# Kernel tuning notes

Hardware: AMD Instinct MI355X
Metric: run time of the kernel (lower is better)

The kernel has to match this reference:

```python
import jax, jax.numpy as jnp
import numpy as np

DIM = 1024

def setup_inputs() -> dict:
    key = jax.random.key(0)
    k1, k2, k3, k4, k5 = jax.random.split(key, 5)
    B, Sq, Skv = 8, 2048, 2048
    x = jax.random.normal(k1, (B, Sq, DIM), dtype=jnp.float32)
    context = jax.random.normal(k2, (B, Skv, DIM), dtype=jnp.float32)
    # nn.Linear default init scale ~ uniform; use scaled normal for stability
    s = DIM ** -0.5
    Wq = jax.random.normal(k3, (DIM, DIM), dtype=jnp.float32) * s
    Wk = jax.random.normal(k4, (DIM, DIM), dtype=jnp.float32) * s
    Wv = jax.random.normal(k5, (DIM, DIM), dtype=jnp.float32) * s
    return {"x": x, "context": context, "Wq": Wq, "Wk": Wk, "Wv": Wv}

def reference(x, context, Wq, Wk, Wv):
    # Linear with weight W applied as x @ W.T (torch convention); here W is [out, in]
    q = jnp.einsum('bsd,ed->bse', x, Wq)          # [B, Sq, D]
    k = jnp.einsum('btd,ed->bte', context, Wk)    # [B, Skv, D]
    v = jnp.einsum('btd,ed->bte', context, Wv)    # [B, Skv, D]
    scale = Wq.shape[0] ** -0.5                   # dim ** -0.5 (no head split)
    dots = jnp.einsum('bse,bte->bst', q, k) * scale  # [B, Sq, Skv]
    attn = jax.nn.softmax(dots, axis=-1)
    out = jnp.einsum('bst,bte->bse', attn, v)     # [B, Sq, D]
    return out
```

## Files before the change

### kernel.cpp

```cpp
#include <hip/hip_runtime.h>


typedef unsigned short u16;
typedef __bf16 bf16x8 __attribute__((ext_vector_type(8)));
typedef float f32x4 __attribute__((ext_vector_type(4)));
typedef u16 us8 __attribute__((ext_vector_type(8)));

__device__ __forceinline__ u16 f2bf(float f) {
  unsigned int u = __float_as_uint(f);
  u += 0x7fffu + ((u >> 16) & 1u);
  return (u16)(u >> 16);
}
__device__ __forceinline__ float bf2f(u16 h) {
  return __uint_as_float((unsigned int)h << 16);
}

struct __attribute__((aligned(8))) us4 { u16 x, y, z, w; };

__global__ __launch_bounds__(256) void cvt_all(
    const float4* __restrict__ x, const float4* __restrict__ c,
    const float4* __restrict__ wq, const float4* __restrict__ wk,
    const float4* __restrict__ wv,
    us4* __restrict__ dxc, us4* __restrict__ dw) {
  int i = blockIdx.x * 256 + threadIdx.x;
  const float4* s; us4* d; float sc = 1.0f;
  if (i < 4194304)      { s = x + i;            d = dxc + i; }
  else if (i < 8388608) { s = c + (i - 4194304); d = dxc + i; }
  else {
    int j = i - 8388608;
    if (j < 262144)      { s = wq + j;            sc = 0.03125f; }
    else if (j < 524288) { s = wk + (j - 262144); }
    else                 { s = wv + (j - 524288); }
    d = dw + j;
  }
  float4 v = *s;
  us4 o{f2bf(v.x * sc), f2bf(v.y * sc), f2bf(v.z * sc), f2bf(v.w * sc)};
  *d = o;
}

__device__ __forceinline__ void gload16(const u16* g, u16* l) {
  __builtin_amdgcn_global_load_lds(
      (const __attribute__((address_space(1))) unsigned int*)g,
      (__attribute__((address_space(3))) unsigned int*)l,
      16, 0, 0);
}

template <bool BF16OUT, bool SM>
__global__ __launch_bounds__(512, 2) void gemm_nt(
    const u16* __restrict__ A, const u16* __restrict__ B, void* __restrict__ Cout,
    int lda, int ldb, int ldc, int K,
    long batchA, long batchB, long batchC, int nx, int ny,
    const float2* __restrict__ stats) {
  __shared__ u16 lds[65536];
  __shared__ float rbuf[256];

  const int p    = blockIdx.x;
  const int slab = gridDim.x >> 3;
  const int gid  = (p & 7) * slab + (p >> 3);
  const int bx   = gid % nx;
  const int t2   = gid / nx;
  const int by   = t2 % ny;
  const int z    = t2 / ny;

  const int tid  = threadIdx.x;
  const int lane = tid & 63;
  const int wv   = tid >> 6;

  const u16* Ab = A + (size_t)z * batchA + (size_t)by * 256 * lda;
  const u16* Bb = B + (size_t)z * batchB + (size_t)bx * 256 * ldb;

  const int srow = tid >> 2;
  const int scol = ((tid & 3) ^ ((tid >> 3) & 3)) * 8;

  const u16* gA = Ab + (size_t)srow * lda + scol;
  const u16* gB = Bb + (size_t)srow * ldb + scol;
  const size_t a128 = (size_t)128 * lda, b128 = (size_t)128 * ldb;

  u16* dA = &lds[tid * 8];
  u16* dB = &lds[16384 + tid * 8];

  float mrow0 = 0.f, mrow1 = 0.f;
  if constexpr (SM) {
    const float2* st = stats + (size_t)z * 2048 + by * 256;
    mrow0 = st[srow].x;
    mrow1 = st[srow + 128].x;
    if (tid < 256) rbuf[tid] = st[tid].y;
  }

  const int fr = lane & 15;
  const int xw = (((lane >> 4) ^ ((lane >> 1) & 3)) * 8);
  const int wm = (wv >> 2) * 128;
  const int wn = (wv & 3) * 64;
  const int rA = (wm + fr) * 32 + xw;
  const int rB = (wn + fr) * 32 + xw;

  const unsigned ldsb = (unsigned)(size_t)&lds[0];
  const unsigned bA0 = ldsb + (unsigned)(rA * 2);
  const unsigned bB0 = ldsb + 32768u + (unsigned)(rB * 2);

  f32x4 acc[8][4];
#pragma unroll
  for (int i = 0; i < 8; i++)
#pragma unroll
    for (int j = 0; j < 4; j++) acc[i][j] = (f32x4)0.f;

  const int NTt = K >> 6;

#define STAGE_A(BUF, KT, H) do {                                  \
    const u16* g_ = gA + (size_t)(KT) * 64 + (H) * 32;            \
    u16* d_ = dA + ((BUF) << 15) + (H) * 8192;                    \
    gload16(g_, d_); gload16(g_ + a128, d_ + 4096); } while (0)
#define STAGE_B(BUF, KT, H) do {                                  \
    const u16* g_ = gB + (size_t)(KT) * 64 + (H) * 32;            \
    u16* d_ = dB + ((BUF) << 15) + (H) * 8192;                    \
    gload16(g_, d_); gload16(g_ + b128, d_ + 4096); } while (0)
#define XFORM(BUFO) do { if constexpr (SM) {                      \
    u16* xb_ = dA + (BUFO);                                       \
    _Pragma("unroll")                                             \
    for (int s_ = 0; s_ < 4; s_++) {                              \
      u16* p_ = xb_ + (s_ & 1) * 4096 + (s_ >> 1) * 8192;         \
      const float mm_ = (s_ & 1) ? mrow1 : mrow0;                 \
      us8 v_ = *(us8*)p_;                                         \
      _Pragma("unroll")                                           \
      for (int k_ = 0; k_ < 8; k_++)                              \
        v_[k_] = f2bf(__expf(bf2f(v_[k_]) - mm_));                \
      *(us8*)p_ = v_;                                             \
    }                                                             \
    asm volatile("s_waitcnt lgkmcnt(0)" ::: "memory");            \
  } } while (0)
#define DSR(D, BASE, IMM)                                         \
    asm volatile("ds_read_b128 %0, %1 offset:" #IMM               \
                 : "=v"(D) : "v"(BASE))
#define LGKM(N) do {                                              \
    asm volatile("s_waitcnt lgkmcnt(" #N ")" ::: "memory");       \
    __builtin_amdgcn_sched_barrier(0); } while (0)
#define MFMA16(AR, AV, BV)                                        \
    __builtin_amdgcn_s_setprio(1);                                \
    _Pragma("unroll")                                             \
    for (int mi_ = 0; mi_ < 4; mi_++)                             \
      _Pragma("unroll")                                           \
      for (int ni_ = 0; ni_ < 4; ni_++)                           \
        acc[(AR) + mi_][ni_] = __builtin_amdgcn_mfma_f32_16x16x32_bf16( \
            __builtin_bit_cast(bf16x8, AV[mi_]),                  \
            __builtin_bit_cast(bf16x8, BV[ni_]),                  \
            acc[(AR) + mi_][ni_], 0, 0, 0);                       \
    __builtin_amdgcn_s_setprio(0);

  STAGE_A(0, 0, 0); STAGE_B(0, 0, 0); STAGE_A(0, 0, 1); STAGE_B(0, 0, 1);
  asm volatile("s_waitcnt vmcnt(0)" ::: "memory");
  XFORM(0);
  __builtin_amdgcn_s_barrier();
  __builtin_amdgcn_sched_barrier(0);

  for (int kt = 0; kt < NTt; ++kt) {
    const unsigned bufo = (kt & 1) ? 65536u : 0u;
    const unsigned bA = bA0 + bufo;
    const unsigned bB = bB0 + bufo;
    const int nb = (kt & 1) ^ 1;
    const bool pf = (kt + 1 < NTt);
    f32x4 a0[4], a1[4], b0[4], c0[4], c1[4], d0[4];

    DSR(a0[0], bA, 0);     DSR(a0[1], bA, 1024);
    DSR(a0[2], bA, 2048);  DSR(a0[3], bA, 3072);
    DSR(b0[0], bB, 0);     DSR(b0[1], bB, 1024);
    DSR(b0[2], bB, 2048);  DSR(b0[3], bB, 3072);
    DSR(a1[0], bA, 4096);  DSR(a1[1], bA, 5120);
    DSR(a1[2], bA, 6144);  DSR(a1[3], bA, 7168);
    if (pf) { STAGE_A(nb, kt + 1, 0); STAGE_B(nb, kt + 1, 0);
              STAGE_A(nb, kt + 1, 1); STAGE_B(nb, kt + 1, 1); }

    LGKM(4);
    MFMA16(0, a0, b0)

    DSR(c0[0], bA, 16384); DSR(c0[1], bA, 17408);
    DSR(c0[2], bA, 18432); DSR(c0[3], bA, 19456);
    DSR(d0[0], bB, 16384); DSR(d0[1], bB, 17408);
    DSR(d0[2], bB, 18432); DSR(d0[3], bB, 19456);
    LGKM(8);
    MFMA16(4, a1, b0)

    DSR(c1[0], bA, 20480); DSR(c1[1], bA, 21504);
    DSR(c1[2], bA, 22528); DSR(c1[3], bA, 23552);
    LGKM(4);
    MFMA16(0, c0, d0)
    LGKM(0);
    MFMA16(4, c1, d0)

    if (pf) {
      asm volatile("s_waitcnt vmcnt(0)" ::: "memory");
      XFORM((unsigned)nb << 15);
      __builtin_amdgcn_s_barrier();
      __builtin_amdgcn_sched_barrier(0);
    }
  }

  const size_t cbase = (size_t)z * batchC;
  const int row0 = by * 256 + wm + (lane >> 4) * 4;
  const int col0 = bx * 256 + wn + fr;
#pragma unroll
  for (int mi = 0; mi < 8; mi++) {
#pragma unroll
    for (int i = 0; i < 4; i++) {
      const size_t roff = cbase + (size_t)(row0 + mi * 16 + i) * ldc + col0;
      float rsc = 1.0f;
      if constexpr (SM) rsc = rbuf[wm + (lane >> 4) * 4 + mi * 16 + i];
#pragma unroll
      for (int ni = 0; ni < 4; ni++) {
        float v = acc[mi][ni][i];
        if constexpr (SM) v *= rsc;
        if constexpr (BF16OUT)
          ((u16*)Cout)[roff + ni * 16] = f2bf(v);
        else
          ((float*)Cout)[roff + ni * 16] = v;
      }
    }
  }
#undef STAGE_A
#undef STAGE_B
#undef XFORM
#undef DSR
#undef LGKM
#undef MFMA16
}

__global__ __launch_bounds__(256) void row_stats_bf16(
    const u16* __restrict__ SP, float2* __restrict__ st) {
  const size_t row = blockIdx.x;
  const us8* p = (const us8*)(SP + row * 2048);
  const int t = threadIdx.x;
  us8 raw = p[t];
  float v[8];
#pragma unroll
  for (int i = 0; i < 8; i++) v[i] = bf2f(raw[i]);

  float m = v[0];
#pragma unroll
  for (int i = 1; i < 8; i++) m = fmaxf(m, v[i]);
#pragma unroll
  for (int o = 32; o; o >>= 1) m = fmaxf(m, __shfl_xor(m, o, 64));
  __shared__ float redm[4];
  if ((t & 63) == 0) redm[t >> 6] = m;
  __syncthreads();
  m = fmaxf(fmaxf(redm[0], redm[1]), fmaxf(redm[2], redm[3]));

  float sum = 0.f;
#pragma unroll
  for (int i = 0; i < 8; i++) sum += __expf(v[i] - m);
#pragma unroll
  for (int o = 32; o; o >>= 1) sum += __shfl_xor(sum, o, 64);
  __shared__ float reds[4];
  if ((t & 63) == 0) reds[t >> 6] = sum;
  __syncthreads();
  if (t == 0) {
    sum = reds[0] + reds[1] + reds[2] + reds[3];
    st[row] = make_float2(m, 1.0f / sum);
  }
}

extern "C" void kernel_launch(void* const* d_in, const int* in_sizes, int n_in,
                              void* d_out, int out_size, void* d_ws, size_t ws_size,
                              hipStream_t stream) {
  const float* x   = (const float*)d_in[0];
  const float* ctx = (const float*)d_in[1];
  const float* Wq  = (const float*)d_in[2];
  const float* Wk  = (const float*)d_in[3];
  const float* Wv  = (const float*)d_in[4];
  float* out = (float*)d_out;

  const size_t NT = 8ull * 2048 * 1024;

  u16* wsu  = (u16*)d_ws;
  u16* xbf  = wsu;
  u16* Sbuf = wsu;
  u16* Vt   = wsu + 2 * NT;
  u16* Wqb  = wsu + 3 * NT;
  float2* stats = (float2*)Wqb;
  u16* Qbf = (u16*)d_out;

  dim3 blk(256), gblk(512);

  cvt_all<<<dim3(35840), blk, 0, stream>>>(
      (const float4*)x, (const float4*)ctx, (const float4*)Wq,
      (const float4*)Wk, (const float4*)Wv, (us4*)xbf, (us4*)Wqb);

  gemm_nt<true, false><<<dim3(512), gblk, 0, stream>>>(
      xbf, Wqb, Qbf, 1024, 1024, 1024, 1024,
      (long)NT, 1024L * 1024, (long)NT, 4, 64, nullptr);
  gemm_nt<true, false><<<dim3(256), gblk, 0, stream>>>(
      Wqb + 2 * 1024 * 1024, wsu + NT, Vt, 1024, 1024, 2048, 1024,
      0L, 2048L * 1024, 1024L * 2048, 8, 4, nullptr);

  gemm_nt<true, false><<<dim3(512), gblk, 0, stream>>>(
      Qbf, Qbf + NT, Sbuf, 1024, 1024, 2048, 1024,
      2048L * 1024, 2048L * 1024, 2048L * 2048, 8, 8, nullptr);

  row_stats_bf16<<<dim3(16384), blk, 0, stream>>>(Sbuf, stats);

  gemm_nt<false, true><<<dim3(256), gblk, 0, stream>>>(
      Sbuf, Vt, out, 2048, 2048, 1024, 2048,
      2048L * 2048, 1024L * 2048, 2048L * 1024, 4, 8, stats);
}
```

Measured before the change: 436.0 us.

## Fuse softmax row statistics into QK^T GEMM epilogue and use base-2 exp

```diff
diff --git a/kernel.cpp b/kernel.cpp
--- a/kernel.cpp
+++ b/kernel.cpp
@@ -13,6 +13,9 @@
 }
 __device__ __forceinline__ float bf2f(u16 h) {
   return __uint_as_float((unsigned int)h << 16);
+}
+__device__ __forceinline__ float exp2a(float x) {
+  float r; asm("v_exp_f32 %0, %1" : "=v"(r) : "v"(x)); return r;
 }
 
 struct __attribute__((aligned(8))) us4 { u16 x, y, z, w; };
@@ -28,7 +31,7 @@
   else if (i < 8388608) { s = c + (i - 4194304); d = dxc + i; }
   else {
     int j = i - 8388608;
-    if (j < 262144)      { s = wq + j;            sc = 0.03125f; }
+    if (j < 262144)      { s = wq + j;            sc = 0.04508422f; }
     else if (j < 524288) { s = wk + (j - 262144); }
     else                 { s = wv + (j - 524288); }
     d = dw + j;
@@ -45,13 +48,14 @@
       16, 0, 0);
 }
 
-template <bool BF16OUT, bool SM>
+template <bool BF16OUT, bool SM, bool ST>
 __global__ __launch_bounds__(512, 2) void gemm_nt(
     const u16* __restrict__ A, const u16* __restrict__ B, void* __restrict__ Cout,
     int lda, int ldb, int ldc, int K,
     long batchA, long batchB, long batchC, int nx, int ny,
-    const float2* __restrict__ stats) {
+    float2* __restrict__ pst) {
   __shared__ u16 lds[65536];
+  __shared__ float smax_l[256];
   __shared__ float rbuf[256];
 
   const int p    = blockIdx.x;
@@ -79,14 +83,6 @@
   u16* dA = &lds[tid * 8];
   u16* dB = &lds[16384 + tid * 8];
 
-  float mrow0 = 0.f, mrow1 = 0.f;
-  if constexpr (SM) {
-    const float2* st = stats + (size_t)z * 2048 + by * 256;
-    mrow0 = st[srow].x;
-    mrow1 = st[srow + 128].x;
-    if (tid < 256) rbuf[tid] = st[tid].y;
-  }
-
   const int fr = lane & 15;
   const int xw = (((lane >> 4) ^ ((lane >> 1) & 3)) * 8);
   const int wm = (wv >> 2) * 128;
@@ -105,6 +101,7 @@
     for (int j = 0; j < 4; j++) acc[i][j] = (f32x4)0.f;
 
   const int NTt = K >> 6;
+  float mrow0 = 0.f, mrow1 = 0.f;
 
 #define STAGE_A(BUF, KT, H) do {                                  \
     const u16* g_ = gA + (size_t)(KT) * 64 + (H) * 32;            \
@@ -118,13 +115,18 @@
     u16* xb_ = dA + (BUFO);                                       \
     _Pragma("unroll")                                             \
     for (int s_ = 0; s_ < 4; s_++) {                              \
-      u16* p_ = xb_ + (s_ & 1) * 4096 + (s_ >> 1) * 8192;         \
+      uint4* p_ = (uint4*)(xb_ + (s_ & 1) * 4096 + (s_ >> 1) * 8192); \
       const float mm_ = (s_ & 1) ? mrow1 : mrow0;                 \
-      us8 v_ = *(us8*)p_;                                         \
+      uint4 v_ = *p_;                                             \
+      unsigned w_[4] = {v_.x, v_.y, v_.z, v_.w};                  \
       _Pragma("unroll")                                           \
-      for (int k_ = 0; k_ < 8; k_++)                              \
-        v_[k_] = f2bf(__expf(bf2f(v_[k_]) - mm_));                \
-      *(us8*)p_ = v_;                                             \
+      for (int k_ = 0; k_ < 4; k_++) {                            \
+        float lo_ = exp2a(__uint_as_float(w_[k_] << 16) - mm_);   \
+        float hi_ = exp2a(__uint_as_float(w_[k_] & 0xffff0000u) - mm_); \
+        asm("v_cvt_pk_bf16_f32 %0, %1, %2"                        \
+            : "=v"(w_[k_]) : "v"(lo_), "v"(hi_));                 \
+      }                                                           \
+      *p_ = make_uint4(w_[0], w_[1], w_[2], w_[3]);               \
     }                                                             \
     asm volatile("s_waitcnt lgkmcnt(0)" ::: "memory");            \
   } } while (0)
@@ -147,6 +149,25 @@
     __builtin_amdgcn_s_setprio(0);
 
   STAGE_A(0, 0, 0); STAGE_B(0, 0, 0); STAGE_A(0, 0, 1); STAGE_B(0, 0, 1);
+  if constexpr (SM) {
+    if (tid < 256) {
+      const float2* pg = pst + (((size_t)z * 8 + by) * 256 + tid) * 8;
+      float2 q[8];
+#pragma unroll
+      for (int j = 0; j < 8; j++) q[j] = pg[j];
+      float M = q[0].x;
+#pragma unroll
+      for (int j = 1; j < 8; j++) M = fmaxf(M, q[j].x);
+      float Ssum = 0.f;
+#pragma unroll
+      for (int j = 0; j < 8; j++) Ssum += q[j].y * exp2a(q[j].x - M);
+      smax_l[tid] = M;
+      rbuf[tid] = 1.0f / Ssum;
+    }
+    __syncthreads();
+    mrow0 = smax_l[srow];
+    mrow1 = smax_l[srow + 128];
+  }
   asm volatile("s_waitcnt vmcnt(0)" ::: "memory");
   XFORM(0);
   __builtin_amdgcn_s_barrier();
@@ -197,6 +218,8 @@
   const size_t cbase = (size_t)z * batchC;
   const int row0 = by * 256 + wm + (lane >> 4) * 4;
   const int col0 = bx * 256 + wn + fr;
+  float2* pstl = (float2*)lds;
+  if constexpr (ST) __syncthreads();
 #pragma unroll
   for (int mi = 0; mi < 8; mi++) {
 #pragma unroll
@@ -204,15 +227,43 @@
       const size_t roff = cbase + (size_t)(row0 + mi * 16 + i) * ldc + col0;
       float rsc = 1.0f;
       if constexpr (SM) rsc = rbuf[wm + (lane >> 4) * 4 + mi * 16 + i];
+      float vr[4];
 #pragma unroll
       for (int ni = 0; ni < 4; ni++) {
         float v = acc[mi][ni][i];
         if constexpr (SM) v *= rsc;
-        if constexpr (BF16OUT)
-          ((u16*)Cout)[roff + ni * 16] = f2bf(v);
-        else
+        if constexpr (BF16OUT) {
+          u16 h = f2bf(v);
+          ((u16*)Cout)[roff + ni * 16] = h;
+          vr[ni] = bf2f(h);
+        } else {
           ((float*)Cout)[roff + ni * 16] = v;
+        }
       }
+      if constexpr (ST) {
+        float mx = fmaxf(fmaxf(vr[0], vr[1]), fmaxf(vr[2], vr[3]));
+#pragma unroll
+        for (int o = 1; o <= 8; o <<= 1) mx = fmaxf(mx, __shfl_xor(mx, o, 64));
+        float ls = 0.f;
+#pragma unroll
+        for (int ni = 0; ni < 4; ni++) ls += exp2a(vr[ni] - mx);
+#pragma unroll
+        for (int o = 1; o <= 8; o <<= 1) ls += __shfl_xor(ls, o, 64);
+        if (fr == 0)
+          pstl[(wm + (lane >> 4) * 4 + mi * 16 + i) * 4 + (wv & 3)] =
+              make_float2(mx, ls);
+      }
+    }
+  }
+  if constexpr (ST) {
+    __syncthreads();
+    if (tid < 256) {
+      float2 q0 = pstl[tid * 4], q1 = pstl[tid * 4 + 1];
+      float2 q2 = pstl[tid * 4 + 2], q3 = pstl[tid * 4 + 3];
+      float M = fmaxf(fmaxf(q0.x, q1.x), fmaxf(q2.x, q3.x));
+      float Ssum = q0.y * exp2a(q0.x - M) + q1.y * exp2a(q1.x - M) +
+                   q2.y * exp2a(q2.x - M) + q3.y * exp2a(q3.x - M);
+      pst[(((size_t)z * 8 + by) * 256 + tid) * 8 + bx] = make_float2(M, Ssum);
     }
   }
 #undef STAGE_A
@@ -221,40 +272,6 @@
 #undef DSR
 #undef LGKM
 #undef MFMA16
-}
-
-__global__ __launch_bounds__(256) void row_stats_bf16(
-    const u16* __restrict__ SP, float2* __restrict__ st) {
-  const size_t row = blockIdx.x;
-  const us8* p = (const us8*)(SP + row * 2048);
-  const int t = threadIdx.x;
-  us8 raw = p[t];
-  float v[8];
-#pragma unroll
-  for (int i = 0; i < 8; i++) v[i] = bf2f(raw[i]);
-
-  float m = v[0];
-#pragma unroll
-  for (int i = 1; i < 8; i++) m = fmaxf(m, v[i]);
-#pragma unroll
-  for (int o = 32; o; o >>= 1) m = fmaxf(m, __shfl_xor(m, o, 64));
-  __shared__ float redm[4];
-  if ((t & 63) == 0) redm[t >> 6] = m;
-  __syncthreads();
-  m = fmaxf(fmaxf(redm[0], redm[1]), fmaxf(redm[2], redm[3]));
-
-  float sum = 0.f;
-#pragma unroll
-  for (int i = 0; i < 8; i++) sum += __expf(v[i] - m);
-#pragma unroll
-  for (int o = 32; o; o >>= 1) sum += __shfl_xor(sum, o, 64);
-  __shared__ float reds[4];
-  if ((t & 63) == 0) reds[t >> 6] = sum;
-  __syncthreads();
-  if (t == 0) {
-    sum = reds[0] + reds[1] + reds[2] + reds[3];
-    st[row] = make_float2(m, 1.0f / sum);
-  }
 }
 
 extern "C" void kernel_launch(void* const* d_in, const int* in_sizes, int n_in,
@@ -274,7 +291,7 @@
   u16* Sbuf = wsu;
   u16* Vt   = wsu + 2 * NT;
   u16* Wqb  = wsu + 3 * NT;
-  float2* stats = (float2*)Wqb;
+  float2* pstats = (float2*)Wqb;
   u16* Qbf = (u16*)d_out;
 
   dim3 blk(256), gblk(512);
@@ -283,20 +300,18 @@
       (const float4*)x, (const float4*)ctx, (const float4*)Wq,
       (const float4*)Wk, (const float4*)Wv, (us4*)xbf, (us4*)Wqb);
 
-  gemm_nt<true, false><<<dim3(512), gblk, 0, stream>>>(
+  gemm_nt<true, false, false><<<dim3(512), gblk, 0, stream>>>(
       xbf, Wqb, Qbf, 1024, 1024, 1024, 1024,
       (long)NT, 1024L * 1024, (long)NT, 4, 64, nullptr);
-  gemm_nt<true, false><<<dim3(256), gblk, 0, stream>>>(
+  gemm_nt<true, false, false><<<dim3(256), gblk, 0, stream>>>(
       Wqb + 2 * 1024 * 1024, wsu + NT, Vt, 1024, 1024, 2048, 1024,
       0L, 2048L * 1024, 1024L * 2048, 8, 4, nullptr);
 
-  gemm_nt<true, false><<<dim3(512), gblk, 0, stream>>>(
+  gemm_nt<true, false, true><<<dim3(512), gblk, 0, stream>>>(
       Qbf, Qbf + NT, Sbuf, 1024, 1024, 2048, 1024,
-      2048L * 1024, 2048L * 1024, 2048L * 2048, 8, 8, nullptr);
-
-  row_stats_bf16<<<dim3(16384), blk, 0, stream>>>(Sbuf, stats);
-
-  gemm_nt<false, true><<<dim3(256), gblk, 0, stream>>>(
+      2048L * 1024, 2048L * 1024, 2048L * 2048, 8, 8, pstats);
+
+  gemm_nt<false, true, false><<<dim3(256), gblk, 0, stream>>>(
       Sbuf, Vt, out, 2048, 2048, 1024, 2048,
-      2048L * 2048, 1024L * 2048, 2048L * 1024, 4, 8, stats);
-}
+      2048L * 2048, 1024L * 2048, 2048L * 1024, 4, 8, pstats);
+}
```

Result: no change. 430.5 us (-1.2%).
